# Kernel tuning notes

Measured on AMD Instinct MI355X. Metric: run time of the kernel, lower is better.

The kernel has to match this reference:

```python
import jax, jax.numpy as jnp
import numpy as np

H = 128  # hidden size
I = 256  # input size

def setup_inputs() -> dict:
    key = jax.random.key(0)
    ks = jax.random.split(key, 12)
    s_ih = 1.0 / np.sqrt(H)
    inp = {
        "x": jax.random.normal(ks[0], (256, 512, I), dtype=jnp.float32),
        # PyTorch LSTM params, gate order (i, f, g, o)
        "W_ih": jax.random.uniform(ks[1], (4 * H, I), jnp.float32, -s_ih, s_ih),
        "W_hh": jax.random.uniform(ks[2], (4 * H, H), jnp.float32, -s_ih, s_ih),
        "b_ih": jax.random.uniform(ks[3], (4 * H,), jnp.float32, -s_ih, s_ih),
        "b_hh": jax.random.uniform(ks[4], (4 * H,), jnp.float32, -s_ih, s_ih),
        "W1": jax.random.uniform(ks[5], (64, H), jnp.float32, -1/np.sqrt(H), 1/np.sqrt(H)),
        "b1": jax.random.uniform(ks[6], (64,), jnp.float32, -1/np.sqrt(H), 1/np.sqrt(H)),
        "W2": jax.random.uniform(ks[7], (32, 64), jnp.float32, -1/np.sqrt(64), 1/np.sqrt(64)),
        "b2": jax.random.uniform(ks[8], (32,), jnp.float32, -1/np.sqrt(64), 1/np.sqrt(64)),
        "W3": jax.random.uniform(ks[9], (4, 32), jnp.float32, -1/np.sqrt(32), 1/np.sqrt(32)),
        "b3": jax.random.uniform(ks[10], (4,), jnp.float32, -1/np.sqrt(32), 1/np.sqrt(32)),
    }
    return inp

def _lstm_last_hidden(x, W_ih, W_hh, b_ih, b_hh):
    B = x.shape[0]
    # Precompute input contribution for all timesteps: [B, T, 4H]
    gx = jnp.einsum("bti,gi->btg", x, W_ih) + (b_ih + b_hh)
    gx = jnp.swapaxes(gx, 0, 1)  # [T, B, 4H] for scan over time

    def step(carry, g_x):
        h, c = carry
        gates = g_x + h @ W_hh.T  # [B, 4H]
        i, f, g, o = jnp.split(gates, 4, axis=-1)
        i = jax.nn.sigmoid(i)
        f = jax.nn.sigmoid(f)
        g = jnp.tanh(g)
        o = jax.nn.sigmoid(o)
        c = f * c + i * g
        h = o * jnp.tanh(c)
        return (h, c), None

    h0 = jnp.zeros((B, H), x.dtype)
    (h, _), _ = jax.lax.scan(step, (h0, h0), gx)
    return h  # last-timestep hidden state [B, H]

def reference(x, W_ih, W_hh, b_ih, b_hh, W1, b1, W2, b2, W3, b3):
    h = _lstm_last_hidden(x, W_ih, W_hh, b_ih, b_hh)
    h = jax.nn.relu(h @ W1.T + b1)
    h = jax.nn.relu(h @ W2.T + b2)
    return h @ W3.T + b3  # [B, 4]
```

## Files before the change

kernel.cpp:

```cpp
#include <hip/hip_runtime.h>
#include <hip/hip_bf16.h>


#define TC       64
#define NCHUNK   8
#define BATCH    256
#define TSEQ     512
#define ISZ      256
#define HSZ      128
#define RB       4
#define NBLK     (BATCH / RB)
#define NGB      (2 * TC * 4)
#define HROW     144
#define GX_PER_T 131072
#define GXCH     ((size_t)TC * GX_PER_T)
#define STRT     32768
#define PF       4

typedef __attribute__((ext_vector_type(8))) short short8;
typedef __attribute__((ext_vector_type(4))) float f32x4;

__device__ __forceinline__ void barrier_nodrain() {
    __asm__ __volatile__("s_waitcnt lgkmcnt(0)\n\ts_barrier" ::: "memory");
}
__device__ __forceinline__ void lds_fence() {
    __asm__ __volatile__("s_waitcnt lgkmcnt(0)" ::: "memory");
}

__device__ __forceinline__ float fast_rcp(float x) {
    return __builtin_amdgcn_rcpf(x);
}
__device__ __forceinline__ float sigmoidf_(float x) {
    return fast_rcp(1.0f + __expf(-x));
}
__device__ __forceinline__ float tanhf_(float x) {
    float e = __expf(2.0f * x);
    return 1.0f - 2.0f * fast_rcp(e + 1.0f);
}
__device__ __forceinline__ unsigned short f2bf(float x) {
    union { float f; unsigned u; } v; v.f = x;
    unsigned r = v.u + 0x7fffu + ((v.u >> 16) & 1u);
    return (unsigned short)(r >> 16);
}
__device__ __forceinline__ float bf2f(unsigned short b) {
    union { unsigned u; float f; } v;
    v.u = ((unsigned)b) << 16;
    return v.f;
}
__device__ __forceinline__ unsigned packbf(float lo, float hi) {
    __hip_bfloat162 h2 = __float22bfloat162_rn(make_float2(lo, hi));
    union { __hip_bfloat162 h; unsigned u; } v; v.h = h2;
    return v.u;
}

__global__ __launch_bounds__(512, 2) void fused_kernel(
    const float* __restrict__ x, const float* __restrict__ Wih,
    const float* __restrict__ bih, const float* __restrict__ bhh,
    const float* __restrict__ Whh,
    const unsigned short* __restrict__ gxl, unsigned short* __restrict__ gxg,
    float* __restrict__ hc, int t0, int first, int run_lstm, int run_gemm)
{
    __shared__ __align__(16) char smem[32768];
    const int tid  = threadIdx.x;
    const int w    = tid >> 6;
    const int lane = tid & 63;
    const int n    = lane & 15;
    const int quad = lane >> 4;

    if (blockIdx.x >= NBLK) {
        if (!run_gemm) return;
        short* As = (short*)smem;
        short* Bs = (short*)(smem + 16384);

        const int gb = (int)blockIdx.x - NBLK;
        const int nt = gb & 3;
        const int mt = gb >> 2;
        const int tl = mt >> 1;
        const int b0 = (mt & 1) * 128;
        const int n0 = nt * 128;

        const int mq = w & 1;
        const int nq = w >> 1;

        const int srow = tid >> 2;
        const int skh  = (tid & 3) * 8;
        const float* xrow = x + ((size_t)(b0 + srow) * TSEQ + (size_t)(t0 + tl)) * ISZ + skh;
        const float* wrow = Wih + (size_t)(n0 + srow) * ISZ + skh;

        f32x4 acc[4][2];
#pragma unroll
        for (int mi = 0; mi < 4; ++mi)
#pragma unroll
            for (int ni = 0; ni < 2; ++ni)
                acc[mi][ni] = (f32x4){0.f, 0.f, 0.f, 0.f};

        {
            float4 pa0 = *(const float4*)(xrow);
            float4 pa1 = *(const float4*)(xrow + 4);
            float4 pb0 = *(const float4*)(wrow);
            float4 pb1 = *(const float4*)(wrow + 4);
            *(uint4*)(&As[srow * 32 + skh]) =
                (uint4){packbf(pa0.x, pa0.y), packbf(pa0.z, pa0.w),
                        packbf(pa1.x, pa1.y), packbf(pa1.z, pa1.w)};
            *(uint4*)(&Bs[srow * 32 + skh]) =
                (uint4){packbf(pb0.x, pb0.y), packbf(pb0.z, pb0.w),
                        packbf(pb1.x, pb1.y), packbf(pb1.z, pb1.w)};
        }
        barrier_nodrain();

        for (int ks = 0; ks < 8; ++ks) {
            const int cur = (ks & 1) * 4096;
            const int nxt = 4096 - cur;

            float4 pa0, pa1, pb0, pb1;
            if (ks < 7) {
                pa0 = *(const float4*)(xrow + (ks + 1) * 32);
                pa1 = *(const float4*)(xrow + (ks + 1) * 32 + 4);
                pb0 = *(const float4*)(wrow + (ks + 1) * 32);
                pb1 = *(const float4*)(wrow + (ks + 1) * 32 + 4);
            }

            short8 af[4], bfr[2];
#pragma unroll
            for (int mi = 0; mi < 4; ++mi)
                af[mi] = *(const short8*)(&As[cur + (mq * 64 + mi * 16 + n) * 32 + quad * 8]);
#pragma unroll
            for (int ni = 0; ni < 2; ++ni)
                bfr[ni] = *(const short8*)(&Bs[cur + (nq * 32 + ni * 16 + n) * 32 + quad * 8]);
#pragma unroll
            for (int mi = 0; mi < 4; ++mi)
#pragma unroll
                for (int ni = 0; ni < 2; ++ni)
                    acc[mi][ni] = __builtin_amdgcn_mfma_f32_16x16x32_bf16(
                        af[mi], bfr[ni], acc[mi][ni], 0, 0, 0);

            if (ks < 7) {
                *(uint4*)(&As[nxt + srow * 32 + skh]) =
                    (uint4){packbf(pa0.x, pa0.y), packbf(pa0.z, pa0.w),
                            packbf(pa1.x, pa1.y), packbf(pa1.z, pa1.w)};
                *(uint4*)(&Bs[nxt + srow * 32 + skh]) =
                    (uint4){packbf(pb0.x, pb0.y), packbf(pb0.z, pb0.w),
                            packbf(pb1.x, pb1.y), packbf(pb1.z, pb1.w)};
            }
            barrier_nodrain();
        }

#pragma unroll
        for (int ni = 0; ni < 2; ++ni) {
            const int j    = nq * 32 + ni * 16 + n;
            const int gate = n0 + j;
            const float bias = bih[gate] + bhh[gate];
            const int wj = nq * 2 + ni;
#pragma unroll
            for (int mi = 0; mi < 4; ++mi) {
                const int bb   = b0 + mq * 64 + mi * 16 + quad * 4;
                const int blk2 = bb >> 2;
                const size_t idx = ((((size_t)nt * TC + tl) * 64 + blk2) * 512) +
                                   (size_t)wj * 64 + (size_t)n * 4;
                const unsigned lo = packbf(acc[mi][ni][0] + bias, acc[mi][ni][1] + bias);
                const unsigned hi = packbf(acc[mi][ni][2] + bias, acc[mi][ni][3] + bias);
                *(uint2*)(&gxg[idx]) = (uint2){lo, hi};
            }
        }
        return;
    }

    if (!run_lstm) return;
    __builtin_amdgcn_s_setprio(1);
    short* h_lds  = (short*)smem;
    float* ex_lds = (float*)(smem + 2304);

    const int blk = (int)blockIdx.x;
    const int b0  = blk * RB;
    const int nb  = lane & 3;
    const int jl  = lane >> 2;
    const int j   = 16 * w + jl;
    float* exw = ex_lds + w * 256;

    short8 Af[4][4];
#pragma unroll
    for (int g = 0; g < 4; ++g) {
        const float* row = Whh + (size_t)(128 * g + 16 * w + n) * HSZ + 8 * quad;
#pragma unroll
        for (int ks = 0; ks < 4; ++ks)
#pragma unroll
            for (int i = 0; i < 8; ++i)
                Af[g][ks][i] = (short)f2bf(row[32 * ks + i]);
    }

    float c1 = 0.f, hl1 = 0.f;
    {
        unsigned short h0 = 0;
        if (!first) {
            c1 = hc[(size_t)BATCH * HSZ + (size_t)(b0 + nb) * HSZ + j];
            h0 = f2bf(hc[(size_t)(b0 + nb) * HSZ + j]);
        }
        *(unsigned short*)&h_lds[nb * HROW + j] = h0;
    }

    const unsigned short* gp[4];
#pragma unroll
    for (int g = 0; g < 4; ++g)
        gp[g] = gxl + (((size_t)g * TC) * 64 + blk) * 512 + (size_t)w * 64 + lane;

    unsigned short gq[PF][4];
#pragma unroll
    for (int d = 0; d < PF; ++d)
#pragma unroll
        for (int g = 0; g < 4; ++g)
            gq[d][g] = gp[g][(size_t)d * STRT];

    barrier_nodrain();

    for (int t = 0; t < TC; t += PF) {
#pragma unroll
        for (int u = 0; u < PF; ++u) {
            const int tt = t + u;
            const short* hb_r = h_lds + (u & 1) * (RB * HROW);
            short*       hb_w = h_lds + ((u & 1) ^ 1) * (RB * HROW);

            short8 Bf[4];
#pragma unroll
            for (int ks = 0; ks < 4; ++ks)
                Bf[ks] = *(const short8*)(&hb_r[nb * HROW + 32 * ks + 8 * quad]);

            const int tf = (tt + PF < TC) ? (tt + PF) : (TC - 1);
            unsigned short gnew[4];
#pragma unroll
            for (int g = 0; g < 4; ++g)
                gnew[g] = gp[g][(size_t)tf * STRT];

            f32x4 acc[4];
#pragma unroll
            for (int g = 0; g < 4; ++g)
                acc[g] = __builtin_amdgcn_mfma_f32_16x16x32_bf16(
                    Af[g][0], Bf[0], (f32x4){0.f, 0.f, 0.f, 0.f}, 0, 0, 0);
#pragma unroll
            for (int ks = 1; ks < 4; ++ks)
#pragma unroll
                for (int g = 0; g < 4; ++g)
                    acc[g] = __builtin_amdgcn_mfma_f32_16x16x32_bf16(
                        Af[g][ks], Bf[ks], acc[g], 0, 0, 0);

            if (n < 4) {
#pragma unroll
                for (int g = 0; g < 4; ++g)
                    *(f32x4*)(&exw[(g * 4 + n) * 16 + 4 * quad]) = acc[g];
            }
            lds_fence();

            const float d0 = exw[(0 * 4 + nb) * 16 + jl];
            const float d1 = exw[(1 * 4 + nb) * 16 + jl];
            const float d2 = exw[(2 * 4 + nb) * 16 + jl];
            const float d3 = exw[(3 * 4 + nb) * 16 + jl];

            const float ig = sigmoidf_(d0 + bf2f(gq[u][0]));
            const float fg = sigmoidf_(d1 + bf2f(gq[u][1]));
            const float gg = tanhf_(d2 + bf2f(gq[u][2]));
            const float og = sigmoidf_(d3 + bf2f(gq[u][3]));
            c1  = fg * c1 + ig * gg;
            hl1 = og * tanhf_(c1);
#pragma unroll
            for (int g = 0; g < 4; ++g) gq[u][g] = gnew[g];

            *(unsigned short*)&hb_w[nb * HROW + j] = f2bf(hl1);
            barrier_nodrain();
        }
    }

    hc[(size_t)(b0 + nb) * HSZ + j] = hl1;
    hc[(size_t)BATCH * HSZ + (size_t)(b0 + nb) * HSZ + j] = c1;
}

__global__ __launch_bounds__(64) void head_kernel(
    const float* __restrict__ hc,
    const float* __restrict__ W1, const float* __restrict__ b1,
    const float* __restrict__ W2, const float* __restrict__ b2,
    const float* __restrict__ W3, const float* __restrict__ b3,
    float* __restrict__ out)
{
    __shared__ float hs[HSZ];
    __shared__ float o1[64];
    __shared__ float o2[32];
    const int bidx = blockIdx.x;
    const int t = threadIdx.x;
    hs[t]      = hc[bidx * HSZ + t];
    hs[t + 64] = hc[bidx * HSZ + t + 64];
    __syncthreads();
    {
        float a = b1[t];
#pragma unroll 8
        for (int k = 0; k < HSZ; ++k) a += W1[t * HSZ + k] * hs[k];
        o1[t] = fmaxf(a, 0.0f);
    }
    __syncthreads();
    if (t < 32) {
        float a = b2[t];
#pragma unroll 8
        for (int k = 0; k < 64; ++k) a += W2[t * 64 + k] * o1[k];
        o2[t] = fmaxf(a, 0.0f);
    }
    __syncthreads();
    if (t < 4) {
        float a = b3[t];
#pragma unroll
        for (int k = 0; k < 32; ++k) a += W3[t * 32 + k] * o2[k];
        out[bidx * 4 + t] = a;
    }
}

extern "C" void kernel_launch(void* const* d_in, const int* in_sizes, int n_in,
                              void* d_out, int out_size, void* d_ws, size_t ws_size,
                              hipStream_t stream) {
    const float* x   = (const float*)d_in[0];
    const float* Wih = (const float*)d_in[1];
    const float* Whh = (const float*)d_in[2];
    const float* bih = (const float*)d_in[3];
    const float* bhh = (const float*)d_in[4];
    const float* W1  = (const float*)d_in[5];
    const float* b1  = (const float*)d_in[6];
    const float* W2  = (const float*)d_in[7];
    const float* b2  = (const float*)d_in[8];
    const float* W3  = (const float*)d_in[9];
    const float* b3  = (const float*)d_in[10];
    float* out = (float*)d_out;

    unsigned short* gx0 = (unsigned short*)d_ws;
    unsigned short* gx1 = gx0 + GXCH;
    float* hc = (float*)((char*)d_ws + 2 * GXCH * sizeof(unsigned short));

    fused_kernel<<<dim3(NBLK + NGB), 512, 0, stream>>>(
        x, Wih, bih, bhh, Whh, gx0, gx0, hc, 0, 1, 0, 1);

    for (int c = 0; c < NCHUNK; ++c) {
        unsigned short* gl = (c & 1) ? gx1 : gx0;
        unsigned short* gg = (c & 1) ? gx0 : gx1;
        fused_kernel<<<dim3(NBLK + NGB), 512, 0, stream>>>(
            x, Wih, bih, bhh, Whh, gl, gg, hc,
            (c + 1) * TC, c == 0 ? 1 : 0, 1, (c + 1) < NCHUNK ? 1 : 0);
    }

    head_kernel<<<dim3(BATCH), 64, 0, stream>>>(hc, W1, b1, W2, b2, W3, b3, out);
}
```

Baseline: 618.0 us.

## Pre-convert inputs to bf16 and read LSTM gate sums straight from MFMA registers

```diff
diff --git a/kernel.cpp b/kernel.cpp
--- a/kernel.cpp
+++ b/kernel.cpp
@@ -17,14 +17,16 @@
 #define STRT     32768
 #define PF       4
 
+#define XN       (BATCH * TSEQ * ISZ)
+#define WIHN     (4 * HSZ * ISZ)
+#define WHHN     (4 * HSZ * HSZ)
+#define NCB      ((XN + WIHN + WHHN) / 8192)
+
 typedef __attribute__((ext_vector_type(8))) short short8;
 typedef __attribute__((ext_vector_type(4))) float f32x4;
 
 __device__ __forceinline__ void barrier_nodrain() {
     __asm__ __volatile__("s_waitcnt lgkmcnt(0)\n\ts_barrier" ::: "memory");
-}
-__device__ __forceinline__ void lds_fence() {
-    __asm__ __volatile__("s_waitcnt lgkmcnt(0)" ::: "memory");
 }
 
 __device__ __forceinline__ float fast_rcp(float x) {
@@ -51,6 +53,11 @@
     __hip_bfloat162 h2 = __float22bfloat162_rn(make_float2(lo, hi));
     union { __hip_bfloat162 h; unsigned u; } v; v.h = h2;
     return v.u;
+}
+__device__ __forceinline__ float sel4(f32x4 v, int r) {
+    float s01 = (r & 1) ? v[1] : v[0];
+    float s23 = (r & 1) ? v[3] : v[2];
+    return (r & 2) ? s23 : s01;
 }
 
 __global__ __launch_bounds__(512, 2) void fused_kernel(
@@ -58,7 +65,10 @@
     const float* __restrict__ bih, const float* __restrict__ bhh,
     const float* __restrict__ Whh,
     const unsigned short* __restrict__ gxl, unsigned short* __restrict__ gxg,
-    float* __restrict__ hc, int t0, int first, int run_lstm, int run_gemm)
+    float* __restrict__ hc,
+    unsigned short* __restrict__ xb, unsigned short* __restrict__ wihb,
+    unsigned short* __restrict__ whhb,
+    int t0, int first, int run_lstm, int run_gemm, int use_xbf, int run_conv)
 {
     __shared__ __align__(16) char smem[32768];
     const int tid  = threadIdx.x;
@@ -67,6 +77,25 @@
     const int n    = lane & 15;
     const int quad = lane >> 4;
 
+    if (blockIdx.x >= NBLK + NGB) {
+        if (!run_conv) return;
+        const int cb = (int)blockIdx.x - (NBLK + NGB);
+        const size_t e0 = ((size_t)cb * 512 + tid) * 16;
+        const float* s; unsigned short* d;
+        if (e0 < (size_t)XN)              { s = x + e0;                d = xb + e0; }
+        else if (e0 < (size_t)(XN + WIHN)){ s = Wih + (e0 - XN);       d = wihb + (e0 - XN); }
+        else                              { s = Whh + (e0 - XN - WIHN); d = whhb + (e0 - XN - WIHN); }
+        float4 f0 = *(const float4*)(s);
+        float4 f1 = *(const float4*)(s + 4);
+        float4 f2 = *(const float4*)(s + 8);
+        float4 f3 = *(const float4*)(s + 12);
+        *(uint4*)(d)     = (uint4){packbf(f0.x, f0.y), packbf(f0.z, f0.w),
+                                   packbf(f1.x, f1.y), packbf(f1.z, f1.w)};
+        *(uint4*)(d + 8) = (uint4){packbf(f2.x, f2.y), packbf(f2.z, f2.w),
+                                   packbf(f3.x, f3.y), packbf(f3.z, f3.w)};
+        return;
+    }
+
     if (blockIdx.x >= NBLK) {
         if (!run_gemm) return;
         short* As = (short*)smem;
@@ -84,8 +113,6 @@
 
         const int srow = tid >> 2;
         const int skh  = (tid & 3) * 8;
-        const float* xrow = x + ((size_t)(b0 + srow) * TSEQ + (size_t)(t0 + tl)) * ISZ + skh;
-        const float* wrow = Wih + (size_t)(n0 + srow) * ISZ + skh;
 
         f32x4 acc[4][2];
 #pragma unroll
@@ -94,55 +121,88 @@
             for (int ni = 0; ni < 2; ++ni)
                 acc[mi][ni] = (f32x4){0.f, 0.f, 0.f, 0.f};
 
-        {
-            float4 pa0 = *(const float4*)(xrow);
-            float4 pa1 = *(const float4*)(xrow + 4);
-            float4 pb0 = *(const float4*)(wrow);
-            float4 pb1 = *(const float4*)(wrow + 4);
-            *(uint4*)(&As[srow * 32 + skh]) =
-                (uint4){packbf(pa0.x, pa0.y), packbf(pa0.z, pa0.w),
-                        packbf(pa1.x, pa1.y), packbf(pa1.z, pa1.w)};
-            *(uint4*)(&Bs[srow * 32 + skh]) =
-                (uint4){packbf(pb0.x, pb0.y), packbf(pb0.z, pb0.w),
-                        packbf(pb1.x, pb1.y), packbf(pb1.z, pb1.w)};
-        }
-        barrier_nodrain();
-
-        for (int ks = 0; ks < 8; ++ks) {
-            const int cur = (ks & 1) * 4096;
-            const int nxt = 4096 - cur;
-
-            float4 pa0, pa1, pb0, pb1;
-            if (ks < 7) {
-                pa0 = *(const float4*)(xrow + (ks + 1) * 32);
-                pa1 = *(const float4*)(xrow + (ks + 1) * 32 + 4);
-                pb0 = *(const float4*)(wrow + (ks + 1) * 32);
-                pb1 = *(const float4*)(wrow + (ks + 1) * 32 + 4);
+        if (use_xbf) {
+            const unsigned short* xr = xb + ((size_t)(b0 + srow) * TSEQ + (size_t)(t0 + tl)) * ISZ + skh;
+            const unsigned short* wr = wihb + (size_t)(n0 + srow) * ISZ + skh;
+            *(short8*)(&As[srow * 32 + skh]) = *(const short8*)(xr);
+            *(short8*)(&Bs[srow * 32 + skh]) = *(const short8*)(wr);
+            barrier_nodrain();
+            for (int ks = 0; ks < 8; ++ks) {
+                const int cur = (ks & 1) * 4096;
+                const int nxt = 4096 - cur;
+                short8 va, vb;
+                if (ks < 7) {
+                    va = *(const short8*)(xr + (ks + 1) * 32);
+                    vb = *(const short8*)(wr + (ks + 1) * 32);
+                }
+                short8 af[4], bfr[2];
+#pragma unroll
+                for (int mi = 0; mi < 4; ++mi)
+                    af[mi] = *(const short8*)(&As[cur + (mq * 64 + mi * 16 + n) * 32 + quad * 8]);
+#pragma unroll
+                for (int ni = 0; ni < 2; ++ni)
+                    bfr[ni] = *(const short8*)(&Bs[cur + (nq * 32 + ni * 16 + n) * 32 + quad * 8]);
+#pragma unroll
+                for (int mi = 0; mi < 4; ++mi)
+#pragma unroll
+                    for (int ni = 0; ni < 2; ++ni)
+                        acc[mi][ni] = __builtin_amdgcn_mfma_f32_16x16x32_bf16(
+                            af[mi], bfr[ni], acc[mi][ni], 0, 0, 0);
+                if (ks < 7) {
+                    *(short8*)(&As[nxt + srow * 32 + skh]) = va;
+                    *(short8*)(&Bs[nxt + srow * 32 + skh]) = vb;
+                }
+                barrier_nodrain();
             }
-
-            short8 af[4], bfr[2];
-#pragma unroll
-            for (int mi = 0; mi < 4; ++mi)
-                af[mi] = *(const short8*)(&As[cur + (mq * 64 + mi * 16 + n) * 32 + quad * 8]);
-#pragma unroll
-            for (int ni = 0; ni < 2; ++ni)
-                bfr[ni] = *(const short8*)(&Bs[cur + (nq * 32 + ni * 16 + n) * 32 + quad * 8]);
-#pragma unroll
-            for (int mi = 0; mi < 4; ++mi)
-#pragma unroll
-                for (int ni = 0; ni < 2; ++ni)
-                    acc[mi][ni] = __builtin_amdgcn_mfma_f32_16x16x32_bf16(
-                        af[mi], bfr[ni], acc[mi][ni], 0, 0, 0);
-
-            if (ks < 7) {
-                *(uint4*)(&As[nxt + srow * 32 + skh]) =
+        } else {
+            const float* xrow = x + ((size_t)(b0 + srow) * TSEQ + (size_t)(t0 + tl)) * ISZ + skh;
+            const float* wrow = Wih + (size_t)(n0 + srow) * ISZ + skh;
+            {
+                float4 pa0 = *(const float4*)(xrow);
+                float4 pa1 = *(const float4*)(xrow + 4);
+                float4 pb0 = *(const float4*)(wrow);
+                float4 pb1 = *(const float4*)(wrow + 4);
+                *(uint4*)(&As[srow * 32 + skh]) =
                     (uint4){packbf(pa0.x, pa0.y), packbf(pa0.z, pa0.w),
                             packbf(pa1.x, pa1.y), packbf(pa1.z, pa1.w)};
-                *(uint4*)(&Bs[nxt + srow * 32 + skh]) =
+                *(uint4*)(&Bs[srow * 32 + skh]) =
                     (uint4){packbf(pb0.x, pb0.y), packbf(pb0.z, pb0.w),
                             packbf(pb1.x, pb1.y), packbf(pb1.z, pb1.w)};
             }
             barrier_nodrain();
+            for (int ks = 0; ks < 8; ++ks) {
+                const int cur = (ks & 1) * 4096;
+                const int nxt = 4096 - cur;
+                float4 pa0, pa1, pb0, pb1;
+                if (ks < 7) {
+                    pa0 = *(const float4*)(xrow + (ks + 1) * 32);
+                    pa1 = *(const float4*)(xrow + (ks + 1) * 32 + 4);
+                    pb0 = *(const float4*)(wrow + (ks + 1) * 32);
+                    pb1 = *(const float4*)(wrow + (ks + 1) * 32 + 4);
+                }
+                short8 af[4], bfr[2];
+#pragma unroll
+                for (int mi = 0; mi < 4; ++mi)
+                    af[mi] = *(const short8*)(&As[cur + (mq * 64 + mi * 16 + n) * 32 + quad * 8]);
+#pragma unroll
+                for (int ni = 0; ni < 2; ++ni)
+                    bfr[ni] = *(const short8*)(&Bs[cur + (nq * 32 + ni * 16 + n) * 32 + quad * 8]);
+#pragma unroll
+                for (int mi = 0; mi < 4; ++mi)
+#pragma unroll
+                    for (int ni = 0; ni < 2; ++ni)
+                        acc[mi][ni] = __builtin_amdgcn_mfma_f32_16x16x32_bf16(
+                            af[mi], bfr[ni], acc[mi][ni], 0, 0, 0);
+                if (ks < 7) {
+                    *(uint4*)(&As[nxt + srow * 32 + skh]) =
+                        (uint4){packbf(pa0.x, pa0.y), packbf(pa0.z, pa0.w),
+                                packbf(pa1.x, pa1.y), packbf(pa1.z, pa1.w)};
+                    *(uint4*)(&Bs[nxt + srow * 32 + skh]) =
+                        (uint4){packbf(pb0.x, pb0.y), packbf(pb0.z, pb0.w),
+                                packbf(pb1.x, pb1.y), packbf(pb1.z, pb1.w)};
+                }
+                barrier_nodrain();
+            }
         }
 
 #pragma unroll
@@ -167,25 +227,22 @@
 
     if (!run_lstm) return;
     __builtin_amdgcn_s_setprio(1);
-    short* h_lds  = (short*)smem;
-    float* ex_lds = (float*)(smem + 2304);
-
-    const int blk = (int)blockIdx.x;
-    const int b0  = blk * RB;
-    const int nb  = lane & 3;
-    const int jl  = lane >> 2;
-    const int j   = 16 * w + jl;
-    float* exw = ex_lds + w * 256;
+    short* h_lds = (short*)smem;
+
+    const int blk  = (int)blockIdx.x;
+    const int b0   = blk * RB;
+    const int nb   = lane & 3;
+    const int jl   = lane >> 2;
+    const int j    = 16 * w + jl;
+    const int rsel = jl & 3;
 
     short8 Af[4][4];
 #pragma unroll
     for (int g = 0; g < 4; ++g) {
-        const float* row = Whh + (size_t)(128 * g + 16 * w + n) * HSZ + 8 * quad;
+        const unsigned short* rowb = whhb + (size_t)(128 * g + 16 * w + n) * HSZ + 8 * quad;
 #pragma unroll
         for (int ks = 0; ks < 4; ++ks)
-#pragma unroll
-            for (int i = 0; i < 8; ++i)
-                Af[g][ks][i] = (short)f2bf(row[32 * ks + i]);
+            Af[g][ks] = *(const short8*)(rowb + 32 * ks);
     }
 
     float c1 = 0.f, hl1 = 0.f;
@@ -224,12 +281,6 @@
             for (int ks = 0; ks < 4; ++ks)
                 Bf[ks] = *(const short8*)(&hb_r[nb * HROW + 32 * ks + 8 * quad]);
 
-            const int tf = (tt + PF < TC) ? (tt + PF) : (TC - 1);
-            unsigned short gnew[4];
-#pragma unroll
-            for (int g = 0; g < 4; ++g)
-                gnew[g] = gp[g][(size_t)tf * STRT];
-
             f32x4 acc[4];
 #pragma unroll
             for (int g = 0; g < 4; ++g)
@@ -242,26 +293,22 @@
                     acc[g] = __builtin_amdgcn_mfma_f32_16x16x32_bf16(
                         Af[g][ks], Bf[ks], acc[g], 0, 0, 0);
 
-            if (n < 4) {
-#pragma unroll
-                for (int g = 0; g < 4; ++g)
-                    *(f32x4*)(&exw[(g * 4 + n) * 16 + 4 * quad]) = acc[g];
-            }
-            lds_fence();
-
-            const float d0 = exw[(0 * 4 + nb) * 16 + jl];
-            const float d1 = exw[(1 * 4 + nb) * 16 + jl];
-            const float d2 = exw[(2 * 4 + nb) * 16 + jl];
-            const float d3 = exw[(3 * 4 + nb) * 16 + jl];
-
-            const float ig = sigmoidf_(d0 + bf2f(gq[u][0]));
-            const float fg = sigmoidf_(d1 + bf2f(gq[u][1]));
-            const float gg = tanhf_(d2 + bf2f(gq[u][2]));
-            const float og = sigmoidf_(d3 + bf2f(gq[u][3]));
+            const float s0 = sel4(acc[0], rsel) + bf2f(gq[u][0]);
+            const float s1 = sel4(acc[1], rsel) + bf2f(gq[u][1]);
+            const float s2 = sel4(acc[2], rsel) + bf2f(gq[u][2]);
+            const float s3 = sel4(acc[3], rsel) + bf2f(gq[u][3]);
+
+            const int tf = (tt + PF < TC) ? (tt + PF) : (TC - 1);
+#pragma unroll
+            for (int g = 0; g < 4; ++g)
+                gq[u][g] = gp[g][(size_t)tf * STRT];
+
+            const float ig = sigmoidf_(s0);
+            const float fg = sigmoidf_(s1);
+            const float gg = tanhf_(s2);
+            const float og = sigmoidf_(s3);
             c1  = fg * c1 + ig * gg;
             hl1 = og * tanhf_(c1);
-#pragma unroll
-            for (int g = 0; g < 4; ++g) gq[u][g] = gnew[g];
 
             *(unsigned short*)&hb_w[nb * HROW + j] = f2bf(hl1);
             barrier_nodrain();
@@ -325,19 +372,24 @@
     const float* b3  = (const float*)d_in[10];
     float* out = (float*)d_out;
 
+    const size_t GXB = GXCH * sizeof(unsigned short);
     unsigned short* gx0 = (unsigned short*)d_ws;
-    unsigned short* gx1 = gx0 + GXCH;
-    float* hc = (float*)((char*)d_ws + 2 * GXCH * sizeof(unsigned short));
-
-    fused_kernel<<<dim3(NBLK + NGB), 512, 0, stream>>>(
-        x, Wih, bih, bhh, Whh, gx0, gx0, hc, 0, 1, 0, 1);
+    unsigned short* gx1 = (unsigned short*)((char*)d_ws + GXB);
+    float* hc = (float*)((char*)d_ws + 2 * GXB);
+    unsigned short* xb   = (unsigned short*)((char*)d_ws + 2 * GXB + 262144);
+    unsigned short* wihb = xb + (size_t)XN;
+    unsigned short* whhb = wihb + WIHN;
+
+    fused_kernel<<<dim3(NBLK + NGB + NCB), 512, 0, stream>>>(
+        x, Wih, bih, bhh, Whh, gx0, gx0, hc, xb, wihb, whhb,
+        0, 1, 0, 1, 0, 1);
 
     for (int c = 0; c < NCHUNK; ++c) {
         unsigned short* gl = (c & 1) ? gx1 : gx0;
         unsigned short* gg = (c & 1) ? gx0 : gx1;
         fused_kernel<<<dim3(NBLK + NGB), 512, 0, stream>>>(
-            x, Wih, bih, bhh, Whh, gl, gg, hc,
-            (c + 1) * TC, c == 0 ? 1 : 0, 1, (c + 1) < NCHUNK ? 1 : 0);
+            x, Wih, bih, bhh, Whh, gl, gg, hc, xb, wihb, whhb,
+            (c + 1) * TC, c == 0 ? 1 : 0, 1, (c + 1) < NCHUNK ? 1 : 0, 1, 0);
     }
 
     head_kernel<<<dim3(BATCH), 64, 0, stream>>>(hc, W1, b1, W2, b2, W3, b3, out);
```

Result: faster. 555.4 us (-10.1%).
